# Performance work log

Measured on AMD Instinct MI355X. Metric: run time of the kernel, lower is better.

## Reference

```python
import jax, jax.numpy as jnp
import numpy as np

EPS = 1e-12  # F.normalize default eps

def setup_inputs() -> dict:
    key = jax.random.key(0)
    ks = jax.random.split(key, 8)
    nq, lq, nd, ld, H, E = 64, 32, 256, 180, 768, 128
    return {
        "query_hidden": jax.random.normal(ks[0], (nq, lq, H), jnp.float32),
        "doc_hidden": jax.random.normal(ks[1], (nd, ld, H), jnp.float32),
        "query_mask": jax.random.randint(ks[2], (nq, lq), 0, 2, jnp.int32).at[:, 0].set(1),
        "doc_punct_mask": jax.random.randint(ks[3], (nd, ld), 0, 2, jnp.int32).at[:, 0].set(1),
        "W1": jax.random.normal(ks[4], (H, H), jnp.float32) * (1.0 / np.sqrt(H)),
        "b1": jnp.zeros((H,), jnp.float32),
        "W2": jax.random.normal(ks[5], (H, E), jnp.float32) * (1.0 / np.sqrt(H)),
        "b2": jnp.zeros((E,), jnp.float32),
    }

def _head(h, W1, b1, W2, b2):
    # embedding_head: Linear -> ReLU -> (Dropout, eval) -> Linear
    return jax.nn.relu(h @ W1 + b1) @ W2 + b2

def _l2norm(x):
    n = jnp.linalg.norm(x, axis=-1, keepdims=True)
    return x / jnp.maximum(n, EPS)

def reference(query_hidden, doc_hidden, query_mask, doc_punct_mask, W1, b1, W2, b2):
    qm = query_mask.astype(jnp.float32)          # [nq, lq]
    dm = doc_punct_mask.astype(jnp.float32)      # [nd, ld]
    # query(): project, mask, L2-normalize per token
    qe = _l2norm(_head(query_hidden, W1, b1, W2, b2) * qm[..., None])  # [nq, lq, E]
    # doc(): project, punctuation-mask, L2-normalize per token
    de = _l2norm(_head(doc_hidden, W1, b1, W2, b2) * dm[..., None])    # [nd, ld, E]
    # score_cart: full cartesian MaxSim
    scores = jnp.einsum('qih,djh->qidj', qe, de)  # [nq, lq, nd, ld]
    masked = scores * dm[None, None, :, :]
    # max over doc tokens, sum over query tokens, normalize by query length
    s = masked.max(axis=-1).sum(axis=1) / qm.sum(axis=-1, keepdims=True)  # [nq, nd]
    return s
```

## Files before the change

kernel.cpp:

```cpp
#include <hip/hip_runtime.h>
#include <hip/hip_bf16.h>

#define H_DIM 768
#define E_DIM 128
#define NQ 64
#define LQ 32
#define ND 256
#define LD 180
#define QTOK (NQ*LQ)
#define DTOK (ND*LD)
#define TTOK (QTOK+DTOK)

typedef __attribute__((ext_vector_type(8))) short short8;
typedef __attribute__((ext_vector_type(4))) float f32x4;
typedef __attribute__((ext_vector_type(4))) float float4v;

__device__ __forceinline__ unsigned short f2bf(float f) {
    union { float f; unsigned u; } v;
    v.f = f;
    unsigned r = v.u + 0x7fffu + ((v.u >> 16) & 1u);
    return (unsigned short)(r >> 16);
}

__device__ __forceinline__ void gl_lds16(const void* g, void* l) {
    __builtin_amdgcn_global_load_lds(
        (const __attribute__((address_space(1))) unsigned char*)g,
        (__attribute__((address_space(3))) unsigned char*)l, 16, 0, 0);
}

__global__ __launch_bounds__(256) void prep_kernel(
    const float* __restrict__ qh, const float* __restrict__ dh,
    const float* __restrict__ W1, const float* __restrict__ W2,
    const int* __restrict__ qmask,
    unsigned short* __restrict__ W1T, unsigned short* __restrict__ W2T,
    float* __restrict__ qcnt, unsigned short* __restrict__ xbf2)
{
    int tid = blockIdx.x * 256 + threadIdx.x;
    int nth = gridDim.x * 256;
    for (int o = tid; o < H_DIM * H_DIM; o += nth) {
        int c = o / H_DIM, k = o - c * H_DIM;
        W1T[o] = f2bf(W1[(size_t)k * H_DIM + c]);
    }
    for (int o = tid; o < E_DIM * H_DIM; o += nth) {
        int c = o / H_DIM, k = o - c * H_DIM;
        W2T[o] = f2bf(W2[(size_t)k * E_DIM + c]);
    }
    if (tid < NQ) {
        int s = 0;
        for (int i = 0; i < LQ; ++i) s += qmask[tid * LQ + i];
        qcnt[tid] = (float)s;
    }
    if (xbf2) {
        const int NSLOT = (TTOK / 16) * 12 * 128;
        for (int S = tid; S < NSLOT; S += nth) {
            int sic = S & 127;
            int chunk = S >> 7;
            int kb = chunk % 12;
            int g  = chunk / 12;
            int ks  = sic >> 6;
            int lh2 = (sic >> 4) & 3;
            int L   = sic & 15;
            int row = g * 16 + L;
            int k0  = kb * 64 + ks * 32 + lh2 * 8;
            const float* src = (row < QTOK)
                ? (qh + (size_t)row * H_DIM + k0)
                : (dh + (size_t)(row - QTOK) * H_DIM + k0);
            float4v a = ((const float4v*)src)[0];
            float4v b = ((const float4v*)src)[1];
            union { unsigned short u[8]; short8 s8; } t;
            t.u[0] = f2bf(a.x); t.u[1] = f2bf(a.y); t.u[2] = f2bf(a.z); t.u[3] = f2bf(a.w);
            t.u[4] = f2bf(b.x); t.u[5] = f2bf(b.y); t.u[6] = f2bf(b.z); t.u[7] = f2bf(b.w);
            *(short8*)(xbf2 + (size_t)S * 8) = t.s8;
        }
    }
}

__global__ __launch_bounds__(256, 4) void head_kernel(
    const float* __restrict__ qh, const float* __restrict__ dh,
    const int* __restrict__ qmv, const int* __restrict__ dmv,
    const float* __restrict__ b1, const float* __restrict__ b2,
    const unsigned short* __restrict__ W1T, const unsigned short* __restrict__ W2T,
    unsigned short* __restrict__ emb, const unsigned short* __restrict__ xbf2)
{
    __shared__ char lds[32768];
    char* Bbuf = lds;
    char* T1   = lds + 16384;

    const int tid = threadIdx.x, lane = tid & 63, wv = tid >> 6;
    const int wm = wv >> 1, wn = wv & 1;
    const int l15 = lane & 15, lhi = lane >> 4;
    const int t0 = blockIdx.x * 64;
    const float* xsrc = (t0 < QTOK) ? (qh + (size_t)t0 * H_DIM)
                                    : (dh + (size_t)(t0 - QTOK) * H_DIM);

    int bcol[4], bk[4];
    #pragma unroll
    for (int i = 0; i < 4; ++i) {
        int o = i * 4096 + wv * 1024 + lane * 16;
        int col = o >> 7;
        bcol[i] = col;
        bk[i] = ((o & 127) ^ ((col & 7) << 4)) >> 1;
    }

    #define STAGE_W1(JB, KB) do {                                              \
        _Pragma("unroll")                                                      \
        for (int i_ = 0; i_ < 4; ++i_)                                         \
            gl_lds16(W1T + (size_t)((JB)*128 + bcol[i_]) * H_DIM + (KB)*64 + bk[i_], \
                     Bbuf + i_*4096 + wv*1024);                                \
    } while (0)
    #define STAGE_W2(JB, HH) do {                                              \
        _Pragma("unroll")                                                      \
        for (int i_ = 0; i_ < 4; ++i_)                                         \
            gl_lds16(W2T + (size_t)bcol[i_] * H_DIM + (JB)*128 + (HH)*64 + bk[i_], \
                     Bbuf + i_*4096 + wv*1024);                                \
    } while (0)

    const f32x4 zero4 = {0.f, 0.f, 0.f, 0.f};
    f32x4 eacc[2][4];
    #pragma unroll
    for (int mt = 0; mt < 2; ++mt)
        #pragma unroll
        for (int nt = 0; nt < 4; ++nt) eacc[mt][nt] = zero4;

    #pragma unroll 1
    for (int jb = 0; jb < 6; ++jb) {
        f32x4 pacc[2][4];
        #pragma unroll
        for (int mt = 0; mt < 2; ++mt)
            #pragma unroll
            for (int nt = 0; nt < 4; ++nt) pacc[mt][nt] = zero4;

        #pragma unroll 1
        for (int kb = 0; kb < 12; ++kb) {
            __syncthreads();
            STAGE_W1(jb, kb);

            short8 afx[2][2];
            if (xbf2) {
                #pragma unroll
                for (int mt = 0; mt < 2; ++mt)
                    #pragma unroll
                    for (int ks = 0; ks < 2; ++ks) {
                        size_t r16 = (size_t)(t0 >> 4) + wm * 2 + mt;
                        afx[mt][ks] = *(const short8*)(xbf2 +
                            ((r16 * 12 + kb) * 2 + ks) * 512 + lhi * 128 + l15 * 8);
                    }
            } else {
                #pragma unroll
                for (int mt = 0; mt < 2; ++mt)
                    #pragma unroll
                    for (int ks = 0; ks < 2; ++ks) {
                        const float* p = xsrc + (size_t)(wm*32 + mt*16 + l15) * H_DIM + kb*64 + ks*32 + lhi*8;
                        float4v a = ((const float4v*)p)[0], b = ((const float4v*)p)[1];
                        union { unsigned short u[8]; short8 s8; } tt;
                        tt.u[0]=f2bf(a.x); tt.u[1]=f2bf(a.y); tt.u[2]=f2bf(a.z); tt.u[3]=f2bf(a.w);
                        tt.u[4]=f2bf(b.x); tt.u[5]=f2bf(b.y); tt.u[6]=f2bf(b.z); tt.u[7]=f2bf(b.w);
                        afx[mt][ks] = tt.s8;
                    }
            }
            __syncthreads();

            #pragma unroll
            for (int ks = 0; ks < 2; ++ks) {
                short8 bfr[4];
                #pragma unroll
                for (int nt = 0; nt < 4; ++nt) {
                    int col = wn * 64 + nt * 16 + l15;
                    int byte = (col * 128 + (ks * 32 + lhi * 8) * 2) ^ ((col & 7) << 4);
                    bfr[nt] = *(const short8*)(Bbuf + byte);
                }
                #pragma unroll
                for (int nt = 0; nt < 4; ++nt)
                    #pragma unroll
                    for (int mt = 0; mt < 2; ++mt)
                        pacc[mt][nt] = __builtin_amdgcn_mfma_f32_16x16x32_bf16(
                            bfr[nt], afx[mt][ks], pacc[mt][nt], 0, 0, 0);
            }
        }

        #pragma unroll
        for (int mt = 0; mt < 2; ++mt) {
            int token = wm * 32 + mt * 16 + l15;
            int sw = (token & 7) << 4;
            #pragma unroll
            for (int nt = 0; nt < 4; ++nt) {
                int c0 = wn * 64 + nt * 16 + lhi * 4;
                union { unsigned short u[4]; unsigned long long q; } pk;
                #pragma unroll
                for (int r = 0; r < 4; ++r) {
                    float v = pacc[mt][nt][r] + b1[jb * 128 + c0 + r];
                    v = v > 0.f ? v : 0.f;
                    pk.u[r] = f2bf(v);
                }
                int byte = (token * 256 + c0 * 2) ^ sw;
                *(unsigned long long*)(T1 + byte) = pk.q;
            }
        }

        #pragma unroll 1
        for (int h = 0; h < 2; ++h) {
            __syncthreads();
            STAGE_W2(jb, h);
            __syncthreads();
            #pragma unroll
            for (int ks = 0; ks < 2; ++ks) {
                short8 at[2], bw[4];
                #pragma unroll
                for (int mt = 0; mt < 2; ++mt) {
                    int row = wm * 32 + mt * 16 + l15;
                    int byte = (row * 256 + (h * 64 + ks * 32 + lhi * 8) * 2) ^ ((row & 7) << 4);
                    at[mt] = *(const short8*)(T1 + byte);
                }
                #pragma unroll
                for (int nt = 0; nt < 4; ++nt) {
                    int col = wn * 64 + nt * 16 + l15;
                    int byte = (col * 128 + (ks * 32 + lhi * 8) * 2) ^ ((col & 7) << 4);
                    bw[nt] = *(const short8*)(Bbuf + byte);
                }
                #pragma unroll
                for (int mt = 0; mt < 2; ++mt)
                    #pragma unroll
                    for (int nt = 0; nt < 4; ++nt)
                        eacc[mt][nt] = __builtin_amdgcn_mfma_f32_16x16x32_bf16(
                            at[mt], bw[nt], eacc[mt][nt], 0, 0, 0);
            }
        }
    }

    float* rs = (float*)lds;
    float b2v[4];
    #pragma unroll
    for (int nt = 0; nt < 4; ++nt) b2v[nt] = b2[wn*64 + nt*16 + l15];

    float vals[2][4][4], sq[2][4];
    #pragma unroll
    for (int mt = 0; mt < 2; ++mt)
        #pragma unroll
        for (int r = 0; r < 4; ++r) {
            int ri = mt*16 + lhi*4 + r;
            int t = t0 + wm*32 + ri;
            float fm = (float)((t < QTOK) ? qmv[t] : dmv[t - QTOK]);
            float s = 0.f;
            #pragma unroll
            for (int nt = 0; nt < 4; ++nt) {
                float v = (eacc[mt][nt][r] + b2v[nt]) * fm;
                vals[mt][nt][r] = v;
                s += v * v;
            }
            sq[mt][r] = s;
        }
    #pragma unroll
    for (int m1 = 1; m1 < 16; m1 <<= 1)
        #pragma unroll
        for (int mt = 0; mt < 2; ++mt)
            #pragma unroll
            for (int r = 0; r < 4; ++r)
                sq[mt][r] += __shfl_xor(sq[mt][r], m1, 64);
    __syncthreads();
    if (l15 == 0) {
        #pragma unroll
        for (int mt = 0; mt < 2; ++mt)
            #pragma unroll
            for (int r = 0; r < 4; ++r)
                rs[wv*32 + mt*16 + lhi*4 + r] = sq[mt][r];
    }
    __syncthreads();
    #pragma unroll
    for (int mt = 0; mt < 2; ++mt)
        #pragma unroll
        for (int r = 0; r < 4; ++r) {
            int ri = mt*16 + lhi*4 + r;
            float tot = rs[(wm*2)*32 + ri] + rs[(wm*2+1)*32 + ri];
            float sc = 1.f / fmaxf(sqrtf(tot), 1e-12f);
            int t = t0 + wm*32 + ri;
            #pragma unroll
            for (int nt = 0; nt < 4; ++nt)
                emb[(size_t)t * E_DIM + wn*64 + nt*16 + l15] = f2bf(vals[mt][nt][r] * sc);
        }
    #undef STAGE_W1
    #undef STAGE_W2
}

__global__ __launch_bounds__(256, 3) void score_kernel(
    const unsigned short* __restrict__ emb, const int* __restrict__ dmask,
    const float* __restrict__ qcnt, float* __restrict__ out)
{
    __shared__ char slds[16384 + 64];
    char* De = slds;
    float* red = (float*)(slds + 16384);

    const int d = blockIdx.x & 255;
    const int qg = blockIdx.x >> 8;
    const int tid = threadIdx.x, lane = tid & 63, wv = tid >> 6;
    const int l15 = lane & 15, lhi = lane >> 4;
    const int srow = tid >> 2, sseg = tid & 3;

    short8 af[4][4];
    #pragma unroll
    for (int mt = 0; mt < 4; ++mt)
        #pragma unroll
        for (int ks = 0; ks < 4; ++ks)
            af[mt][ks] = *(const short8*)(emb +
                (size_t)(qg*256 + wv*64 + mt*16 + l15) * E_DIM + ks*32 + lhi*8);

    float rmax[4][4];
    #pragma unroll
    for (int mt = 0; mt < 4; ++mt)
        #pragma unroll
        for (int r = 0; r < 4; ++r) rmax[mt][r] = -3.0e38f;

    const f32x4 zero4 = {0.f, 0.f, 0.f, 0.f};
    for (int ch = 0; ch < 3; ++ch) {
        int j = ch*64 + srow;
        int jv = (j < LD) ? j : 0;
        const unsigned short* src = emb + (size_t)(QTOK + d*LD + jv) * E_DIM + sseg*32;
        if (ch) __syncthreads();
        #pragma unroll
        for (int i = 0; i < 4; ++i) {
            short8 v = *(const short8*)(src + i*8);
            int byte = (srow * 256 + (sseg*32 + i*8) * 2) ^ ((srow & 7) << 4);
            *(short8*)(De + byte) = v;
        }
        __syncthreads();
        #pragma unroll
        for (int nt = 0; nt < 4; ++nt) {
            short8 bfr[4];
            int col = nt*16 + l15;
            #pragma unroll
            for (int ks = 0; ks < 4; ++ks) {
                int byte = (col * 256 + (ks*32 + lhi*8) * 2) ^ ((col & 7) << 4);
                bfr[ks] = *(const short8*)(De + byte);
            }
            f32x4 acc[4] = {zero4, zero4, zero4, zero4};
            #pragma unroll
            for (int ks = 0; ks < 4; ++ks)
                #pragma unroll
                for (int mt = 0; mt < 4; ++mt)
                    acc[mt] = __builtin_amdgcn_mfma_f32_16x16x32_bf16(
                        af[mt][ks], bfr[ks], acc[mt], 0, 0, 0);
            int jcol = ch*64 + nt*16 + l15;
            float mval = (jcol < LD) ? (float)dmask[d*LD + jcol] : -1.f;
            #pragma unroll
            for (int mt = 0; mt < 4; ++mt)
                #pragma unroll
                for (int r = 0; r < 4; ++r) {
                    float v = (mval < 0.f) ? -3.0e38f : acc[mt][r] * mval;
                    rmax[mt][r] = fmaxf(rmax[mt][r], v);
                }
        }
    }
    #pragma unroll
    for (int m1 = 1; m1 < 16; m1 <<= 1)
        #pragma unroll
        for (int mt = 0; mt < 4; ++mt)
            #pragma unroll
            for (int r = 0; r < 4; ++r)
                rmax[mt][r] = fmaxf(rmax[mt][r], __shfl_xor(rmax[mt][r], m1, 64));
    float s0 = 0.f, s1 = 0.f;
    #pragma unroll
    for (int r = 0; r < 4; ++r) { s0 += rmax[0][r] + rmax[1][r]; s1 += rmax[2][r] + rmax[3][r]; }
    s0 += __shfl_xor(s0, 16, 64); s0 += __shfl_xor(s0, 32, 64);
    s1 += __shfl_xor(s1, 16, 64); s1 += __shfl_xor(s1, 32, 64);
    if (lane == 0) { red[wv*2 + 0] = s0; red[wv*2 + 1] = s1; }
    __syncthreads();
    if (tid < 8) {
        int q = qg*8 + tid;
        out[q * ND + d] = red[tid] / qcnt[q];
    }
}

extern "C" void kernel_launch(void* const* d_in, const int* in_sizes, int n_in,
                              void* d_out, int out_size, void* d_ws, size_t ws_size,
                              hipStream_t stream)
{
    const float* qh = (const float*)d_in[0];
    const float* dh = (const float*)d_in[1];
    const int*   qm = (const int*)d_in[2];
    const int*   dm = (const int*)d_in[3];
    const float* W1 = (const float*)d_in[4];
    const float* b1 = (const float*)d_in[5];
    const float* W2 = (const float*)d_in[6];
    const float* b2 = (const float*)d_in[7];
    float* out = (float*)d_out;

    unsigned short* emb = (unsigned short*)d_ws;
    unsigned short* W1T = emb + (size_t)TTOK * E_DIM;
    unsigned short* W2T = W1T + (size_t)H_DIM * H_DIM;
    float* qcnt = (float*)(W2T + (size_t)E_DIM * H_DIM);
    size_t base_need = (size_t)TTOK*E_DIM*2 + (size_t)H_DIM*H_DIM*2
                     + (size_t)E_DIM*H_DIM*2 + 256;
    size_t xbf_need = (size_t)TTOK * H_DIM * 2;
    unsigned short* xbf2 = nullptr;
    if (ws_size >= base_need + xbf_need)
        xbf2 = (unsigned short*)((char*)d_ws + base_need);

    prep_kernel<<<2048, 256, 0, stream>>>(qh, dh, W1, W2, qm, W1T, W2T, qcnt, xbf2);
    head_kernel<<<TTOK / 64, 256, 0, stream>>>(qh, dh, qm, dm, b1, b2, W1T, W2T, emb, xbf2);
    score_kernel<<<8 * ND, 256, 0, stream>>>(emb, dm, qcnt, out);
}
```

Before: 217.0 us.

## Double K-tile depth in head GEMM and prefetch activation fragments

Widens the staged weight tile from 64 to 128 K-elements, doubling the LDS buffer, so each W1 phase uses 6 iterations instead of 12 and W2 is staged in one pass instead of two. This halves the number of barrier pairs per output block. The pre-converted bf16 activation fragments are now loaded one K-step ahead in registers, interleaved with the MFMAs, to hide global latency. In exchange, LDS grows to 48KB, the occupancy hint drops from 4 to 3 blocks, and register pressure rises.

```diff
diff --git a/kernel.cpp b/kernel.cpp
--- a/kernel.cpp
+++ b/kernel.cpp
@@ -75,16 +75,16 @@
     }
 }
 
-__global__ __launch_bounds__(256, 4) void head_kernel(
+__global__ __launch_bounds__(256, 3) void head_kernel(
     const float* __restrict__ qh, const float* __restrict__ dh,
     const int* __restrict__ qmv, const int* __restrict__ dmv,
     const float* __restrict__ b1, const float* __restrict__ b2,
     const unsigned short* __restrict__ W1T, const unsigned short* __restrict__ W2T,
     unsigned short* __restrict__ emb, const unsigned short* __restrict__ xbf2)
 {
-    __shared__ char lds[32768];
+    __shared__ char lds[49152];
     char* Bbuf = lds;
-    char* T1   = lds + 16384;
+    char* T1   = lds + 32768;
 
     const int tid = threadIdx.x, lane = tid & 63, wv = tid >> 6;
     const int wm = wv >> 1, wn = wv & 1;
@@ -93,25 +93,25 @@
     const float* xsrc = (t0 < QTOK) ? (qh + (size_t)t0 * H_DIM)
                                     : (dh + (size_t)(t0 - QTOK) * H_DIM);
 
-    int bcol[4], bk[4];
-    #pragma unroll
-    for (int i = 0; i < 4; ++i) {
+    int bcol[8], bk[8];
+    #pragma unroll
+    for (int i = 0; i < 8; ++i) {
         int o = i * 4096 + wv * 1024 + lane * 16;
-        int col = o >> 7;
+        int col = o >> 8;
         bcol[i] = col;
-        bk[i] = ((o & 127) ^ ((col & 7) << 4)) >> 1;
-    }
-
-    #define STAGE_W1(JB, KB) do {                                              \
+        bk[i] = ((o & 255) ^ ((col & 7) << 4)) >> 1;
+    }
+
+    #define STAGE_W1(JB, KB2) do {                                             \
         _Pragma("unroll")                                                      \
-        for (int i_ = 0; i_ < 4; ++i_)                                         \
-            gl_lds16(W1T + (size_t)((JB)*128 + bcol[i_]) * H_DIM + (KB)*64 + bk[i_], \
+        for (int i_ = 0; i_ < 8; ++i_)                                         \
+            gl_lds16(W1T + (size_t)((JB)*128 + bcol[i_]) * H_DIM + (KB2)*128 + bk[i_], \
                      Bbuf + i_*4096 + wv*1024);                                \
     } while (0)
-    #define STAGE_W2(JB, HH) do {                                              \
+    #define STAGE_W2(JB) do {                                                  \
         _Pragma("unroll")                                                      \
-        for (int i_ = 0; i_ < 4; ++i_)                                         \
-            gl_lds16(W2T + (size_t)bcol[i_] * H_DIM + (JB)*128 + (HH)*64 + bk[i_], \
+        for (int i_ = 0; i_ < 8; ++i_)                                         \
+            gl_lds16(W2T + (size_t)bcol[i_] * H_DIM + (JB)*128 + bk[i_],       \
                      Bbuf + i_*4096 + wv*1024);                                \
     } while (0)
 
@@ -121,6 +121,18 @@
     for (int mt = 0; mt < 2; ++mt)
         #pragma unroll
         for (int nt = 0; nt < 4; ++nt) eacc[mt][nt] = zero4;
+
+    const size_t r16b = (size_t)(t0 >> 4);
+
+    short8 afx[2][4];
+    if (xbf2) {
+        #pragma unroll
+        for (int mt = 0; mt < 2; ++mt)
+            #pragma unroll
+            for (int ks = 0; ks < 4; ++ks)
+                afx[mt][ks] = *(const short8*)(xbf2 +
+                    ((r16b + wm*2 + mt) * 24 + 0*4 + ks) * 512 + lhi*128 + l15*8);
+    }
 
     #pragma unroll 1
     for (int jb = 0; jb < 6; ++jb) {
@@ -131,26 +143,15 @@
             for (int nt = 0; nt < 4; ++nt) pacc[mt][nt] = zero4;
 
         #pragma unroll 1
-        for (int kb = 0; kb < 12; ++kb) {
+        for (int kb2 = 0; kb2 < 6; ++kb2) {
             __syncthreads();
-            STAGE_W1(jb, kb);
-
-            short8 afx[2][2];
-            if (xbf2) {
+            STAGE_W1(jb, kb2);
+            if (!xbf2) {
                 #pragma unroll
                 for (int mt = 0; mt < 2; ++mt)
                     #pragma unroll
-                    for (int ks = 0; ks < 2; ++ks) {
-                        size_t r16 = (size_t)(t0 >> 4) + wm * 2 + mt;
-                        afx[mt][ks] = *(const short8*)(xbf2 +
-                            ((r16 * 12 + kb) * 2 + ks) * 512 + lhi * 128 + l15 * 8);
-                    }
-            } else {
-                #pragma unroll
-                for (int mt = 0; mt < 2; ++mt)
-                    #pragma unroll
-                    for (int ks = 0; ks < 2; ++ks) {
-                        const float* p = xsrc + (size_t)(wm*32 + mt*16 + l15) * H_DIM + kb*64 + ks*32 + lhi*8;
+                    for (int ks = 0; ks < 4; ++ks) {
+                        const float* p = xsrc + (size_t)(wm*32 + mt*16 + l15) * H_DIM + kb2*128 + ks*32 + lhi*8;
                         float4v a = ((const float4v*)p)[0], b = ((const float4v*)p)[1];
                         union { unsigned short u[8]; short8 s8; } tt;
                         tt.u[0]=f2bf(a.x); tt.u[1]=f2bf(a.y); tt.u[2]=f2bf(a.z); tt.u[3]=f2bf(a.w);
@@ -160,13 +161,14 @@
             }
             __syncthreads();
 
-            #pragma unroll
-            for (int ks = 0; ks < 2; ++ks) {
+            const int nkb2 = (kb2 == 5) ? 0 : kb2 + 1;
+            #pragma unroll
+            for (int ks = 0; ks < 4; ++ks) {
                 short8 bfr[4];
                 #pragma unroll
                 for (int nt = 0; nt < 4; ++nt) {
                     int col = wn * 64 + nt * 16 + l15;
-                    int byte = (col * 128 + (ks * 32 + lhi * 8) * 2) ^ ((col & 7) << 4);
+                    int byte = (col * 256 + (ks * 32 + lhi * 8) * 2) ^ ((col & 7) << 4);
                     bfr[nt] = *(const short8*)(Bbuf + byte);
                 }
                 #pragma unroll
@@ -175,6 +177,12 @@
                     for (int mt = 0; mt < 2; ++mt)
                         pacc[mt][nt] = __builtin_amdgcn_mfma_f32_16x16x32_bf16(
                             bfr[nt], afx[mt][ks], pacc[mt][nt], 0, 0, 0);
+                if (xbf2) {
+                    #pragma unroll
+                    for (int mt = 0; mt < 2; ++mt)
+                        afx[mt][ks] = *(const short8*)(xbf2 +
+                            ((r16b + wm*2 + mt) * 24 + nkb2*4 + ks) * 512 + lhi*128 + l15*8);
+                }
             }
         }
 
@@ -197,33 +205,30 @@
             }
         }
 
-        #pragma unroll 1
-        for (int h = 0; h < 2; ++h) {
-            __syncthreads();
-            STAGE_W2(jb, h);
-            __syncthreads();
-            #pragma unroll
-            for (int ks = 0; ks < 2; ++ks) {
-                short8 at[2], bw[4];
-                #pragma unroll
-                for (int mt = 0; mt < 2; ++mt) {
-                    int row = wm * 32 + mt * 16 + l15;
-                    int byte = (row * 256 + (h * 64 + ks * 32 + lhi * 8) * 2) ^ ((row & 7) << 4);
-                    at[mt] = *(const short8*)(T1 + byte);
-                }
-                #pragma unroll
-                for (int nt = 0; nt < 4; ++nt) {
-                    int col = wn * 64 + nt * 16 + l15;
-                    int byte = (col * 128 + (ks * 32 + lhi * 8) * 2) ^ ((col & 7) << 4);
-                    bw[nt] = *(const short8*)(Bbuf + byte);
-                }
-                #pragma unroll
-                for (int mt = 0; mt < 2; ++mt)
-                    #pragma unroll
-                    for (int nt = 0; nt < 4; ++nt)
-                        eacc[mt][nt] = __builtin_amdgcn_mfma_f32_16x16x32_bf16(
-                            at[mt], bw[nt], eacc[mt][nt], 0, 0, 0);
-            }
+        __syncthreads();
+        STAGE_W2(jb);
+        __syncthreads();
+        #pragma unroll
+        for (int ks = 0; ks < 4; ++ks) {
+            short8 at[2], bw[4];
+            #pragma unroll
+            for (int mt = 0; mt < 2; ++mt) {
+                int row = wm * 32 + mt * 16 + l15;
+                int byte = (row * 256 + (ks * 32 + lhi * 8) * 2) ^ ((row & 7) << 4);
+                at[mt] = *(const short8*)(T1 + byte);
+            }
+            #pragma unroll
+            for (int nt = 0; nt < 4; ++nt) {
+                int col = wn * 64 + nt * 16 + l15;
+                int byte = (col * 256 + (ks * 32 + lhi * 8) * 2) ^ ((col & 7) << 4);
+                bw[nt] = *(const short8*)(Bbuf + byte);
+            }
+            #pragma unroll
+            for (int mt = 0; mt < 2; ++mt)
+                #pragma unroll
+                for (int nt = 0; nt < 4; ++nt)
+                    eacc[mt][nt] = __builtin_amdgcn_mfma_f32_16x16x32_bf16(
+                        at[mt], bw[nt], eacc[mt][nt], 0, 0, 0);
         }
     }
 
```

After: 218.7 us. Within noise of the previous version (+0.8%).
